# Kernel optimization log

Measured on AMD Instinct MI355X. Metric: run time of the kernel, lower is better.

## Reference

```python
import jax, jax.numpy as jnp
import numpy as np

B, S, E = 2, 2048, 1024
H, D = 16, 64          # num_heads, head_dim
FF = 4096              # ff_dim = 4*E
EPS = 1e-5


def _layer_norm(x, g, b):
    mu = jnp.mean(x, axis=-1, keepdims=True)
    var = jnp.mean(jnp.square(x - mu), axis=-1, keepdims=True)
    return (x - mu) * jax.lax.rsqrt(var + EPS) * g + b


def setup_inputs() -> dict:
    key = jax.random.key(0)
    ks = jax.random.split(key, 9)
    s = lambda fan_in: 1.0 / np.sqrt(fan_in)
    return {
        "x": jax.random.normal(ks[0], (B, S, E), dtype=jnp.float32),
        "w_qkv": jax.random.uniform(ks[1], (3 * E, E), jnp.float32, -s(E), s(E)),
        "b_qkv": jnp.zeros((3 * E,), jnp.float32),
        "w_out": jax.random.uniform(ks[2], (E, E), jnp.float32, -s(E), s(E)),
        "b_out": jnp.zeros((E,), jnp.float32),
        "g1": jnp.ones((E,), jnp.float32),
        "beta1": jnp.zeros((E,), jnp.float32),
        "w_fc1": jax.random.uniform(ks[3], (FF, E), jnp.float32, -s(E), s(E)),
        "b_fc1": jnp.zeros((FF,), jnp.float32),
        "w_fc2": jax.random.uniform(ks[4], (E, FF), jnp.float32, -s(FF), s(FF)),
        "b_fc2": jnp.zeros((E,), jnp.float32),
        "g2": jnp.ones((E,), jnp.float32),
        "beta2": jnp.zeros((E,), jnp.float32),
    }


def reference(x, w_qkv, b_qkv, w_out, b_out, g1, beta1, w_fc1, b_fc1, w_fc2, b_fc2, g2, beta2):
    scale = 1.0 / np.sqrt(D)
    # QKV projection: [B,S,3E] -> [3,B,H,S,D]
    qkv = (x @ w_qkv.T + b_qkv).reshape(B, S, 3, H, D).transpose(2, 0, 3, 1, 4)
    q, k, v = qkv[0], qkv[1], qkv[2]
    attn = jax.nn.softmax(jnp.einsum('bhqd,bhkd->bhqk', q, k) * scale, axis=-1)
    out = jnp.einsum('bhqk,bhkd->bhqd', attn, v)          # [B,H,S,D]
    out = out.transpose(0, 2, 1, 3).reshape(B, S, E)
    attn_out = out @ w_out.T + b_out
    x1 = _layer_norm(x + attn_out, g1, beta1)
    h = jax.nn.gelu(x1 @ w_fc1.T + b_fc1, approximate=False)  # torch GELU = exact erf
    ff_out = h @ w_fc2.T + b_fc2
    return _layer_norm(x1 + ff_out, g2, beta2)
```

## Files before the change

kernel.cpp:

```cpp
#include <hip/hip_runtime.h>
#include <hip/hip_bf16.h>
#include <math.h>
#include <type_traits>

typedef __hip_bfloat16 bf16;
using short8 = __attribute__((ext_vector_type(8))) short;
using f32x4  = __attribute__((ext_vector_type(4))) float;

#define TS 2048
#define TH 16
#define TD 64
#define TE 1024
#define T3E 3072

__device__ __forceinline__ void gload16(void* lds, const void* g) {
    __builtin_amdgcn_global_load_lds(
        (__attribute__((address_space(1))) void*)g,
        (__attribute__((address_space(3))) void*)lds, 16, 0, 0);
}

__global__ __launch_bounds__(256) void f2b(
    const float* __restrict__ s, bf16* __restrict__ d)
{
    size_t i = ((size_t)blockIdx.x * 256 + threadIdx.x) * 8;
    float4 a = *(const float4*)&s[i];
    float4 b = *(const float4*)&s[i + 4];
    bf16 t[8];
    t[0] = __float2bfloat16(a.x); t[1] = __float2bfloat16(a.y);
    t[2] = __float2bfloat16(a.z); t[3] = __float2bfloat16(a.w);
    t[4] = __float2bfloat16(b.x); t[5] = __float2bfloat16(b.y);
    t[6] = __float2bfloat16(b.z); t[7] = __float2bfloat16(b.w);
    *(uint4*)&d[i] = *(uint4*)t;
}

template <typename TC, bool GELU, bool QS>
__global__ __launch_bounds__(256) void gemm_bt(
    const bf16* __restrict__ A, const bf16* __restrict__ Bw,
    const float* __restrict__ bias, TC* __restrict__ C,
    int M, int N, int K, int kLen)
{
    __shared__ bf16 As[128 * 32];
    __shared__ bf16 Bs[128 * 32];

    const int t    = threadIdx.x;
    const int lane = t & 63;
    const int wave = t >> 6;
    const int wr   = wave >> 1;
    const int wc   = wave & 1;
    const int lr   = lane & 15;
    const int lq   = lane >> 4;
    const int mBase = blockIdx.y * 128;
    const int nBase = blockIdx.x * 128;
    const int kOff  = blockIdx.z * kLen;

    const int srow = lane >> 2;
    const int skc  = (lane & 3) * 8;

    f32x4 acc[4][4];
    #pragma unroll
    for (int mi = 0; mi < 4; mi++)
        #pragma unroll
        for (int ni = 0; ni < 4; ni++)
            acc[mi][ni] = (f32x4){0.f, 0.f, 0.f, 0.f};

    for (int k0 = kOff; k0 < kOff + kLen; k0 += 32) {
        #pragma unroll
        for (int c = 0; c < 2; c++) {
            int r0 = wave * 32 + c * 16;
            gload16(&As[r0 * 32],
                    &A[(size_t)(mBase + r0 + srow) * K + k0 + skc]);
            gload16(&Bs[r0 * 32],
                    &Bw[(size_t)(nBase + r0 + srow) * K + k0 + skc]);
        }
        __syncthreads();

        short8 af[4], bfr[4];
        #pragma unroll
        for (int mi = 0; mi < 4; mi++)
            af[mi] = *(const short8*)&As[(wr * 64 + mi * 16 + lr) * 32 + lq * 8];
        #pragma unroll
        for (int ni = 0; ni < 4; ni++)
            bfr[ni] = *(const short8*)&Bs[(wc * 64 + ni * 16 + lr) * 32 + lq * 8];

        #pragma unroll
        for (int mi = 0; mi < 4; mi++)
            #pragma unroll
            for (int ni = 0; ni < 4; ni++)
                acc[mi][ni] = __builtin_amdgcn_mfma_f32_16x16x32_bf16(
                    af[mi], bfr[ni], acc[mi][ni], 0, 0, 0);
        __syncthreads();
    }

    const size_t cOff = (size_t)blockIdx.z * M * N;
    #pragma unroll
    for (int mi = 0; mi < 4; mi++) {
        #pragma unroll
        for (int ni = 0; ni < 4; ni++) {
            int c = nBase + wc * 64 + ni * 16 + lr;
            float bv = (blockIdx.z == 0) ? bias[c] : 0.f;
            #pragma unroll
            for (int i = 0; i < 4; i++) {
                int r = mBase + wr * 64 + mi * 16 + lq * 4 + i;
                float v = acc[mi][ni][i] + bv;
                if constexpr (GELU)
                    v = 0.5f * v * (1.0f + erff(v * 0.70710678118f));
                if constexpr (QS)
                    if (c < TE) v *= 0.180336880111f;
                if constexpr (std::is_same_v<TC, bf16>)
                    C[cOff + (size_t)r * N + c] = __float2bfloat16(v);
                else
                    C[cOff + (size_t)r * N + c] = v;
            }
        }
    }
}

__global__ __launch_bounds__(256) void vtrans(
    const bf16* __restrict__ qkv, bf16* __restrict__ vT)
{
    __shared__ bf16 T[64 * 72];
    const int t  = threadIdx.x;
    const int s0 = blockIdx.x * 64;
    const int bh = blockIdx.y;
    const int b = bh >> 4, h = bh & 15;
    const size_t srcBase = ((size_t)b * TS + s0) * T3E + 2 * TE + h * TD;

    #pragma unroll
    for (int i = 0; i < 2; i++) {
        int tok = (t >> 3) + i * 32;
        int c   = t & 7;
        int cw  = c ^ ((tok >> 3) & 7);
        *(uint4*)&T[tok * 72 + cw * 8] =
            *(const uint4*)&qkv[srcBase + (size_t)tok * T3E + c * 8];
    }
    __syncthreads();
    #pragma unroll
    for (int i = 0; i < 2; i++) {
        int d   = (t >> 3) + i * 32;
        int sof = (t & 7) * 8;
        bf16 tmp[8];
        #pragma unroll
        for (int j = 0; j < 8; j++) {
            int s = sof + j;
            tmp[j] = T[s * 72 + (((d >> 3) ^ ((s >> 3) & 7)) << 3) + (d & 7)];
        }
        *(uint4*)&vT[((size_t)bh * TD + d) * TS + s0 + sof] = *(uint4*)tmp;
    }
}

#define FA_SK 72
#define FA_SV 136
#define FA_SP 136

__global__ __launch_bounds__(256, 2) void attn_flash(
    const bf16* __restrict__ qkv, const bf16* __restrict__ vT,
    bf16* __restrict__ attnO)
{
    __shared__ bf16 KV[128 * FA_SK];
    __shared__ bf16 Ps[4 * 32 * FA_SP];
    bf16* Ks = KV;
    bf16* Vt = KV;

    const int t    = threadIdx.x;
    const int lane = t & 63;
    const int wv   = t >> 6;
    const int lr   = lane & 15;
    const int lq   = lane >> 4;
    const int qt   = blockIdx.x;
    const int bh   = blockIdx.y;
    const int h = bh & 15, b = bh >> 4;
    const size_t tokBase = (size_t)b * TS;

    bf16* Pw = Ps + wv * 32 * FA_SP;

    short8 qf[2][2];
    #pragma unroll
    for (int mi = 0; mi < 2; mi++)
        #pragma unroll
        for (int kc = 0; kc < 2; kc++)
            qf[mi][kc] = *(const short8*)&qkv[
                (tokBase + qt * 128 + wv * 32 + mi * 16 + lr) * T3E
                + h * TD + kc * 32 + lq * 8];

    f32x4 oacc[2][4];
    f32x4 lacc[2];
    #pragma unroll
    for (int mi = 0; mi < 2; mi++) {
        lacc[mi] = (f32x4){0.f, 0.f, 0.f, 0.f};
        #pragma unroll
        for (int ni = 0; ni < 4; ni++)
            oacc[mi][ni] = (f32x4){0.f, 0.f, 0.f, 0.f};
    }
    const short o1 = (short)0x3F80;
    const short8 ones8 = (lr == 0) ? (short8){o1,o1,o1,o1,o1,o1,o1,o1}
                                   : (short8){0,0,0,0,0,0,0,0};

    const int vd = t >> 2;
    const int vc = (t & 3) * 8;

    for (int it = 0; it < 16; it++) {
        const int kb0 = it * 128;
        __syncthreads();

        #pragma unroll
        for (int i = 0; i < 4; i++) {
            int l  = t + i * 256;
            int r  = l >> 3;
            int ch = (l & 7) * 8;
            *(uint4*)&Ks[r * FA_SK + ch] =
                *(const uint4*)&qkv[(tokBase + kb0 + r) * T3E + TE + h * TD + ch];
        }
        uint4 vreg[4];
        {
            const bf16* vsrc = &vT[((size_t)bh * TD + vd) * TS + kb0 + vc];
            #pragma unroll
            for (int i = 0; i < 4; i++)
                vreg[i] = *(const uint4*)&vsrc[i * 32];
        }
        __syncthreads();

        f32x4 sacc[2][8];
        #pragma unroll
        for (int kc = 0; kc < 2; kc++) {
            short8 kf[8];
            #pragma unroll
            for (int ni = 0; ni < 8; ni++)
                kf[ni] = *(const short8*)&Ks[(ni * 16 + lr) * FA_SK + kc * 32 + lq * 8];
            #pragma unroll
            for (int mi = 0; mi < 2; mi++)
                #pragma unroll
                for (int ni = 0; ni < 8; ni++)
                    sacc[mi][ni] = __builtin_amdgcn_mfma_f32_16x16x32_bf16(
                        qf[mi][kc], kf[ni],
                        kc == 0 ? (f32x4){0.f,0.f,0.f,0.f} : sacc[mi][ni], 0, 0, 0);
        }
        __syncthreads();

        #pragma unroll
        for (int i = 0; i < 4; i++)
            *(uint4*)&Vt[vd * FA_SV + vc + i * 32] = vreg[i];

        #pragma unroll
        for (int mi = 0; mi < 2; mi++) {
            #pragma unroll
            for (int ni = 0; ni < 8; ni++) {
                const int cbase = ni * 2 + (lr >> 3);
                #pragma unroll
                for (int rg = 0; rg < 4; rg++) {
                    float p = exp2f(fminf(sacc[mi][ni][rg], 80.f));
                    const int q  = mi * 16 + lq * 4 + rg;
                    const int cw = cbase ^ (mi * 4 + lq);
                    Pw[q * FA_SP + cw * 8 + (lr & 7)] = __float2bfloat16(p);
                }
            }
        }
        __syncthreads();

        #pragma unroll
        for (int kc = 0; kc < 4; kc++) {
            short8 pa[2], vb[4];
            #pragma unroll
            for (int mi = 0; mi < 2; mi++) {
                const int cw = (kc * 4 + lq) ^ ((mi * 4 + (lr >> 2)) & 7);
                pa[mi] = *(const short8*)&Pw[(mi * 16 + lr) * FA_SP + cw * 8];
            }
            #pragma unroll
            for (int ni = 0; ni < 4; ni++)
                vb[ni] = *(const short8*)&Vt[(ni * 16 + lr) * FA_SV + kc * 32 + lq * 8];
            #pragma unroll
            for (int mi = 0; mi < 2; mi++) {
                lacc[mi] = __builtin_amdgcn_mfma_f32_16x16x32_bf16(
                    pa[mi], ones8, lacc[mi], 0, 0, 0);
                #pragma unroll
                for (int ni = 0; ni < 4; ni++)
                    oacc[mi][ni] = __builtin_amdgcn_mfma_f32_16x16x32_bf16(
                        pa[mi], vb[ni], oacc[mi][ni], 0, 0, 0);
            }
        }
    }

    #pragma unroll
    for (int mi = 0; mi < 2; mi++) {
        float inv[4];
        #pragma unroll
        for (int rg = 0; rg < 4; rg++) {
            float lb = __shfl(lacc[mi][rg], lane & 48, 64);
            inv[rg] = 1.0f / lb;
        }
        #pragma unroll
        for (int ni = 0; ni < 4; ni++) {
            #pragma unroll
            for (int rg = 0; rg < 4; rg++) {
                float o = oacc[mi][ni][rg] * inv[rg];
                attnO[(tokBase + qt * 128 + wv * 32 + mi * 16 + lq * 4 + rg) * TE
                      + h * TD + ni * 16 + lr] = __float2bfloat16(o);
            }
        }
    }
}

__global__ __launch_bounds__(256) void add_ln3(
    const float* __restrict__ a, const float* __restrict__ p0,
    const float* __restrict__ p1, const float* __restrict__ g,
    const float* __restrict__ beta, float* __restrict__ out,
    bf16* __restrict__ outb)
{
    __shared__ float r1[256], r2[256];
    const int t = threadIdx.x;
    const size_t row = (size_t)blockIdx.x * TE;

    float4 va = *(const float4*)&a[row + t * 4];
    float4 v0 = *(const float4*)&p0[row + t * 4];
    float4 v1 = *(const float4*)&p1[row + t * 4];
    float v[4] = {va.x + v0.x + v1.x, va.y + v0.y + v1.y,
                  va.z + v0.z + v1.z, va.w + v0.w + v1.w};
    float s = 0.f, s2 = 0.f;
    #pragma unroll
    for (int i = 0; i < 4; i++) { s += v[i]; s2 += v[i] * v[i]; }
    r1[t] = s; r2[t] = s2;
    __syncthreads();
    for (int off = 128; off > 0; off >>= 1) {
        if (t < off) { r1[t] += r1[t + off]; r2[t] += r2[t + off]; }
        __syncthreads();
    }
    const float mu  = r1[0] * (1.f / 1024.f);
    const float var = r2[0] * (1.f / 1024.f) - mu * mu;
    const float rs  = rsqrtf(var + 1e-5f);
    float4 vg  = *(const float4*)&g[t * 4];
    float4 vbt = *(const float4*)&beta[t * 4];
    float o[4];
    o[0] = (v[0] - mu) * rs * vg.x + vbt.x;
    o[1] = (v[1] - mu) * rs * vg.y + vbt.y;
    o[2] = (v[2] - mu) * rs * vg.z + vbt.z;
    o[3] = (v[3] - mu) * rs * vg.w + vbt.w;
    *(float4*)&out[row + t * 4] = *(float4*)o;
    if (outb) {
        bf16 ob[4];
        #pragma unroll
        for (int i = 0; i < 4; i++) ob[i] = __float2bfloat16(o[i]);
        *(uint2*)&outb[row + t * 4] = *(uint2*)ob;
    }
}

extern "C" void kernel_launch(void* const* d_in, const int* in_sizes, int n_in,
                              void* d_out, int out_size, void* d_ws, size_t ws_size,
                              hipStream_t stream)
{
    const float* x     = (const float*)d_in[0];
    const float* w_qkv = (const float*)d_in[1];
    const float* b_qkv = (const float*)d_in[2];
    const float* w_out = (const float*)d_in[3];
    const float* b_out = (const float*)d_in[4];
    const float* g1    = (const float*)d_in[5];
    const float* beta1 = (const float*)d_in[6];
    const float* w_fc1 = (const float*)d_in[7];
    const float* b_fc1 = (const float*)d_in[8];
    const float* w_fc2 = (const float*)d_in[9];
    const float* b_fc2 = (const float*)d_in[10];
    const float* g2    = (const float*)d_in[11];
    const float* beta2 = (const float*)d_in[12];
    float* out = (float*)d_out;

    char* wsb   = (char*)d_ws;
    bf16*  qkv   = (bf16*)(wsb);
    bf16*  hbuf  = (bf16*)(wsb);
    bf16*  attnO = (bf16*)(wsb + 33554432);
    float* y     = (float*)(wsb + 41943040);
    float* ff    = y;
    bf16*  xb    = (bf16*)(wsb + 75497472);
    bf16*  vT    = (bf16*)(wsb + 75497472);
    float* x1    = (float*)(wsb + 75497472);
    bf16*  x1b   = (bf16*)(wsb + 92274688);
    bf16*  wqkvb = (bf16*)(wsb + 100663296);
    bf16*  woutb = (bf16*)(wsb + 106954752);
    bf16*  wfc1b = (bf16*)(wsb + 109051904);
    bf16*  wfc2b = (bf16*)(wsb + 117440512);

    const int M = 2 * TS;
    const size_t PART = (size_t)M * TE;
    dim3 blk(256);

    f2b<<<dim3(2048), blk, 0, stream>>>(x, xb);
    f2b<<<dim3(1536), blk, 0, stream>>>(w_qkv, wqkvb);
    f2b<<<dim3(512),  blk, 0, stream>>>(w_out, woutb);
    f2b<<<dim3(2048), blk, 0, stream>>>(w_fc1, wfc1b);
    f2b<<<dim3(2048), blk, 0, stream>>>(w_fc2, wfc2b);

    gemm_bt<bf16, false, true><<<dim3(24, 32, 1), blk, 0, stream>>>(
        xb, wqkvb, b_qkv, qkv, M, T3E, TE, TE);
    vtrans<<<dim3(TS / 64, 2 * TH), blk, 0, stream>>>(qkv, vT);
    attn_flash<<<dim3(TS / 128, 2 * TH), blk, 0, stream>>>(qkv, vT, attnO);
    gemm_bt<float, false, false><<<dim3(8, 32, 2), blk, 0, stream>>>(
        attnO, woutb, b_out, y, M, TE, TE, TE / 2);
    add_ln3<<<dim3(M), blk, 0, stream>>>(x, y, y + PART, g1, beta1, x1, x1b);
    gemm_bt<bf16, true, false><<<dim3(32, 32, 1), blk, 0, stream>>>(
        x1b, wfc1b, b_fc1, hbuf, M, 4096, TE, TE);
    gemm_bt<float, false, false><<<dim3(8, 32, 2), blk, 0, stream>>>(
        hbuf, wfc2b, b_fc2, ff, M, TE, 4096, 2048);
    add_ln3<<<dim3(M), blk, 0, stream>>>(x1, ff, ff + PART, g2, beta2, out, nullptr);
}
```

Before: 439.7 us.

## Keep attention probabilities in registers via transposed S and merge weight casts

The attention kernel now computes S transposed (K times Q), so each lane's exp'd scores can be packed straight into bf16 B-operands for a 16x16x16 MFMA against V. This removes the P round-trip through shared memory, the ones-matrix MFMA used for row sums, and two barriers per tile. In exchange, query tiles shrink from 128 to 64 rows (16 per wave) with a higher occupancy target, which doubles the number of K/V tile loads per head. The five fp32-to-bf16 cast launches are also merged into one multi-buffer kernel to cut launch overhead.

```diff
diff --git a/kernel.cpp b/kernel.cpp
--- a/kernel.cpp
+++ b/kernel.cpp
@@ -4,8 +4,9 @@
 #include <type_traits>
 
 typedef __hip_bfloat16 bf16;
-using short8 = __attribute__((ext_vector_type(8))) short;
-using f32x4  = __attribute__((ext_vector_type(4))) float;
+using short8  = __attribute__((ext_vector_type(8))) short;
+using short4v = __attribute__((ext_vector_type(4))) short;
+using f32x4   = __attribute__((ext_vector_type(4))) float;
 
 #define TS 2048
 #define TH 16
@@ -19,10 +20,26 @@
         (__attribute__((address_space(3))) void*)lds, 16, 0, 0);
 }
 
-__global__ __launch_bounds__(256) void f2b(
-    const float* __restrict__ s, bf16* __restrict__ d)
-{
-    size_t i = ((size_t)blockIdx.x * 256 + threadIdx.x) * 8;
+__device__ __forceinline__ uint32_t pkbf16(float a, float b) {
+    return (uint32_t)__bfloat16_as_ushort(__float2bfloat16(a)) |
+           ((uint32_t)__bfloat16_as_ushort(__float2bfloat16(b)) << 16);
+}
+
+__global__ __launch_bounds__(256) void f2b_multi(
+    const float* __restrict__ s0, bf16* __restrict__ d0,
+    const float* __restrict__ s1, bf16* __restrict__ d1,
+    const float* __restrict__ s2, bf16* __restrict__ d2,
+    const float* __restrict__ s3, bf16* __restrict__ d3,
+    const float* __restrict__ s4, bf16* __restrict__ d4)
+{
+    int blk = blockIdx.x;
+    const float* s; bf16* d; int base;
+    if (blk < 2048)      { s = s0; d = d0; base = 0; }
+    else if (blk < 3584) { s = s1; d = d1; base = 2048; }
+    else if (blk < 4096) { s = s2; d = d2; base = 3584; }
+    else if (blk < 6144) { s = s3; d = d3; base = 4096; }
+    else                 { s = s4; d = d4; base = 6144; }
+    size_t i = ((size_t)(blk - base) * 256 + threadIdx.x) * 8;
     float4 a = *(const float4*)&s[i];
     float4 b = *(const float4*)&s[i + 4];
     bf16 t[8];
@@ -148,52 +165,33 @@
     }
 }
 
-#define FA_SK 72
-#define FA_SV 136
-#define FA_SP 136
-
-__global__ __launch_bounds__(256, 2) void attn_flash(
+__global__ __launch_bounds__(256, 4) void attn_flash(
     const bf16* __restrict__ qkv, const bf16* __restrict__ vT,
     bf16* __restrict__ attnO)
 {
-    __shared__ bf16 KV[128 * FA_SK];
-    __shared__ bf16 Ps[4 * 32 * FA_SP];
-    bf16* Ks = KV;
-    bf16* Vt = KV;
+    __shared__ bf16 Ks[128 * 72];
+    __shared__ bf16 Vt[64 * 136];
 
     const int t    = threadIdx.x;
     const int lane = t & 63;
     const int wv   = t >> 6;
-    const int lr   = lane & 15;
-    const int lq   = lane >> 4;
+    const int c    = lane & 15;
+    const int u    = lane >> 4;
     const int qt   = blockIdx.x;
     const int bh   = blockIdx.y;
     const int h = bh & 15, b = bh >> 4;
     const size_t tokBase = (size_t)b * TS;
-
-    bf16* Pw = Ps + wv * 32 * FA_SP;
-
-    short8 qf[2][2];
-    #pragma unroll
-    for (int mi = 0; mi < 2; mi++)
-        #pragma unroll
-        for (int kc = 0; kc < 2; kc++)
-            qf[mi][kc] = *(const short8*)&qkv[
-                (tokBase + qt * 128 + wv * 32 + mi * 16 + lr) * T3E
-                + h * TD + kc * 32 + lq * 8];
-
-    f32x4 oacc[2][4];
-    f32x4 lacc[2];
-    #pragma unroll
-    for (int mi = 0; mi < 2; mi++) {
-        lacc[mi] = (f32x4){0.f, 0.f, 0.f, 0.f};
-        #pragma unroll
-        for (int ni = 0; ni < 4; ni++)
-            oacc[mi][ni] = (f32x4){0.f, 0.f, 0.f, 0.f};
-    }
-    const short o1 = (short)0x3F80;
-    const short8 ones8 = (lr == 0) ? (short8){o1,o1,o1,o1,o1,o1,o1,o1}
-                                   : (short8){0,0,0,0,0,0,0,0};
+    const int qrow = qt * 64 + wv * 16 + c;
+
+    short8 qf[2];
+    #pragma unroll
+    for (int kc = 0; kc < 2; kc++)
+        qf[kc] = *(const short8*)&qkv[(tokBase + qrow) * T3E + h * TD + kc * 32 + u * 8];
+
+    f32x4 oacc[4];
+    #pragma unroll
+    for (int di = 0; di < 4; di++) oacc[di] = (f32x4){0.f, 0.f, 0.f, 0.f};
+    float lsum = 0.f;
 
     const int vd = t >> 2;
     const int vc = (t & 3) * 8;
@@ -204,98 +202,68 @@
 
         #pragma unroll
         for (int i = 0; i < 4; i++) {
-            int l  = t + i * 256;
-            int r  = l >> 3;
-            int ch = (l & 7) * 8;
-            *(uint4*)&Ks[r * FA_SK + ch] =
+            int l = t + i * 256;
+            int r = l >> 3, ch = (l & 7) * 8;
+            *(uint4*)&Ks[r * 72 + ch] =
                 *(const uint4*)&qkv[(tokBase + kb0 + r) * T3E + TE + h * TD + ch];
         }
-        uint4 vreg[4];
         {
-            const bf16* vsrc = &vT[((size_t)bh * TD + vd) * TS + kb0 + vc];
+            const bf16* vs = &vT[((size_t)bh * TD + vd) * TS + kb0 + vc];
             #pragma unroll
             for (int i = 0; i < 4; i++)
-                vreg[i] = *(const uint4*)&vsrc[i * 32];
-        }
-        __syncthreads();
-
-        f32x4 sacc[2][8];
+                *(uint4*)&Vt[vd * 136 + vc + i * 32] = *(const uint4*)&vs[i * 32];
+        }
+        __syncthreads();
+
+        f32x4 sacc[8];
         #pragma unroll
         for (int kc = 0; kc < 2; kc++) {
-            short8 kf[8];
-            #pragma unroll
-            for (int ni = 0; ni < 8; ni++)
-                kf[ni] = *(const short8*)&Ks[(ni * 16 + lr) * FA_SK + kc * 32 + lq * 8];
-            #pragma unroll
-            for (int mi = 0; mi < 2; mi++)
-                #pragma unroll
-                for (int ni = 0; ni < 8; ni++)
-                    sacc[mi][ni] = __builtin_amdgcn_mfma_f32_16x16x32_bf16(
-                        qf[mi][kc], kf[ni],
-                        kc == 0 ? (f32x4){0.f,0.f,0.f,0.f} : sacc[mi][ni], 0, 0, 0);
-        }
-        __syncthreads();
-
-        #pragma unroll
-        for (int i = 0; i < 4; i++)
-            *(uint4*)&Vt[vd * FA_SV + vc + i * 32] = vreg[i];
-
-        #pragma unroll
-        for (int mi = 0; mi < 2; mi++) {
-            #pragma unroll
-            for (int ni = 0; ni < 8; ni++) {
-                const int cbase = ni * 2 + (lr >> 3);
-                #pragma unroll
-                for (int rg = 0; rg < 4; rg++) {
-                    float p = exp2f(fminf(sacc[mi][ni][rg], 80.f));
-                    const int q  = mi * 16 + lq * 4 + rg;
-                    const int cw = cbase ^ (mi * 4 + lq);
-                    Pw[q * FA_SP + cw * 8 + (lr & 7)] = __float2bfloat16(p);
-                }
+            #pragma unroll
+            for (int kb = 0; kb < 8; kb++) {
+                short8 kf = *(const short8*)&Ks[(kb * 16 + c) * 72 + kc * 32 + u * 8];
+                sacc[kb] = __builtin_amdgcn_mfma_f32_16x16x32_bf16(
+                    kf, qf[kc],
+                    kc == 0 ? (f32x4){0.f, 0.f, 0.f, 0.f} : sacc[kb], 0, 0, 0);
             }
         }
-        __syncthreads();
-
-        #pragma unroll
-        for (int kc = 0; kc < 4; kc++) {
-            short8 pa[2], vb[4];
-            #pragma unroll
-            for (int mi = 0; mi < 2; mi++) {
-                const int cw = (kc * 4 + lq) ^ ((mi * 4 + (lr >> 2)) & 7);
-                pa[mi] = *(const short8*)&Pw[(mi * 16 + lr) * FA_SP + cw * 8];
+
+        uint32_t pT[8][2];
+        #pragma unroll
+        for (int kb = 0; kb < 8; kb++) {
+            float p0 = exp2f(fminf(sacc[kb][0], 80.f));
+            float p1 = exp2f(fminf(sacc[kb][1], 80.f));
+            float p2 = exp2f(fminf(sacc[kb][2], 80.f));
+            float p3 = exp2f(fminf(sacc[kb][3], 80.f));
+            lsum += (p0 + p1) + (p2 + p3);
+            pT[kb][0] = pkbf16(p0, p1);
+            pT[kb][1] = pkbf16(p2, p3);
+        }
+
+        #pragma unroll
+        for (int kb = 0; kb < 8; kb++) {
+            union { uint32_t d[2]; short4v s; } pb;
+            pb.d[0] = pT[kb][0];
+            pb.d[1] = pT[kb][1];
+            #pragma unroll
+            for (int di = 0; di < 4; di++) {
+                short4v va = *(const short4v*)&Vt[(di * 16 + c) * 136 + kb * 16 + u * 4];
+                oacc[di] = __builtin_amdgcn_mfma_f32_16x16x16bf16_1k(
+                    va, pb.s, oacc[di], 0, 0, 0);
             }
-            #pragma unroll
-            for (int ni = 0; ni < 4; ni++)
-                vb[ni] = *(const short8*)&Vt[(ni * 16 + lr) * FA_SV + kc * 32 + lq * 8];
-            #pragma unroll
-            for (int mi = 0; mi < 2; mi++) {
-                lacc[mi] = __builtin_amdgcn_mfma_f32_16x16x32_bf16(
-                    pa[mi], ones8, lacc[mi], 0, 0, 0);
-                #pragma unroll
-                for (int ni = 0; ni < 4; ni++)
-                    oacc[mi][ni] = __builtin_amdgcn_mfma_f32_16x16x32_bf16(
-                        pa[mi], vb[ni], oacc[mi][ni], 0, 0, 0);
-            }
-        }
-    }
-
-    #pragma unroll
-    for (int mi = 0; mi < 2; mi++) {
-        float inv[4];
-        #pragma unroll
-        for (int rg = 0; rg < 4; rg++) {
-            float lb = __shfl(lacc[mi][rg], lane & 48, 64);
-            inv[rg] = 1.0f / lb;
-        }
-        #pragma unroll
-        for (int ni = 0; ni < 4; ni++) {
-            #pragma unroll
-            for (int rg = 0; rg < 4; rg++) {
-                float o = oacc[mi][ni][rg] * inv[rg];
-                attnO[(tokBase + qt * 128 + wv * 32 + mi * 16 + lq * 4 + rg) * TE
-                      + h * TD + ni * 16 + lr] = __float2bfloat16(o);
-            }
-        }
+        }
+    }
+
+    lsum += __shfl_xor(lsum, 16, 64);
+    lsum += __shfl_xor(lsum, 32, 64);
+    const float inv = 1.0f / lsum;
+
+    #pragma unroll
+    for (int di = 0; di < 4; di++) {
+        bf16 ob[4];
+        #pragma unroll
+        for (int rg = 0; rg < 4; rg++)
+            ob[rg] = __float2bfloat16(oacc[di][rg] * inv);
+        *(uint2*)&attnO[(tokBase + qrow) * TE + h * TD + di * 16 + u * 4] = *(uint2*)ob;
     }
 }
 
@@ -380,16 +348,13 @@
     const size_t PART = (size_t)M * TE;
     dim3 blk(256);
 
-    f2b<<<dim3(2048), blk, 0, stream>>>(x, xb);
-    f2b<<<dim3(1536), blk, 0, stream>>>(w_qkv, wqkvb);
-    f2b<<<dim3(512),  blk, 0, stream>>>(w_out, woutb);
-    f2b<<<dim3(2048), blk, 0, stream>>>(w_fc1, wfc1b);
-    f2b<<<dim3(2048), blk, 0, stream>>>(w_fc2, wfc2b);
+    f2b_multi<<<dim3(8192), blk, 0, stream>>>(
+        x, xb, w_qkv, wqkvb, w_out, woutb, w_fc1, wfc1b, w_fc2, wfc2b);
 
     gemm_bt<bf16, false, true><<<dim3(24, 32, 1), blk, 0, stream>>>(
         xb, wqkvb, b_qkv, qkv, M, T3E, TE, TE);
     vtrans<<<dim3(TS / 64, 2 * TH), blk, 0, stream>>>(qkv, vT);
-    attn_flash<<<dim3(TS / 128, 2 * TH), blk, 0, stream>>>(qkv, vT, attnO);
+    attn_flash<<<dim3(TS / 64, 2 * TH), blk, 0, stream>>>(qkv, vT, attnO);
     gemm_bt<float, false, false><<<dim3(8, 32, 2), blk, 0, stream>>>(
         attnO, woutb, b_out, y, M, TE, TE, TE / 2);
     add_ln3<<<dim3(M), blk, 0, stream>>>(x, y, y + PART, g1, beta1, x1, x1b);
```

Result: faster. 427.9 us (-2.7%).
